# Optimization experiments

Measured on AMD Instinct MI355X. Metric: run time of the kernel, lower is better.

## Reference

```python
import jax, jax.numpy as jnp
import numpy as np

N = 8192      # number of tree nodes
K = 8         # max degree (8-ary tree)
ALPHA = 64    # alphabet size
DH = 256      # hidden dim


def _lin_w(key, din, dout):
    return jax.random.normal(key, (din, dout), jnp.float32) / np.sqrt(din)


def setup_inputs() -> dict:
    keys = jax.random.split(jax.random.key(0), 24)
    node_types = jax.random.randint(keys[0], (N,), 0, ALPHA, dtype=jnp.int32)
    # deterministic K-ary tree: children of node n are n*K+1 .. n*K+K (if < N)
    idx = np.arange(N)[:, None] * K + 1 + np.arange(K)[None, :]
    mask = idx < N
    children_np = np.where(mask, idx, 0).astype(np.int32)
    A_np = np.zeros((N, N), np.float32)
    A_np[np.repeat(np.arange(N), K)[mask.ravel()], idx.ravel()[mask.ravel()]] = 1.0
    return {
        "node_types": node_types,
        "children": jnp.asarray(children_np),
        "child_mask": jnp.asarray(mask),
        "A": jnp.asarray(A_np),
        # GCN layer params (self-transform + neighbor-transform)
        "Ws0": _lin_w(keys[1], ALPHA, DH), "Wn0": _lin_w(keys[2], ALPHA, DH), "b0": jnp.zeros((DH,), jnp.float32),
        "Ws1": _lin_w(keys[3], DH, DH),    "Wn1": _lin_w(keys[4], DH, DH),    "b1": jnp.zeros((DH,), jnp.float32),
        "Ws2": _lin_w(keys[5], DH, DH),    "Wn2": _lin_w(keys[6], DH, DH),    "b2": jnp.zeros((DH,), jnp.float32),
        # heads
        "we": _lin_w(keys[7], DH, 1), "be": jnp.zeros((1,), jnp.float32),
        "Wt": _lin_w(keys[8], DH, ALPHA), "bt": jnp.zeros((ALPHA,), jnp.float32),
        "ciu_w": _lin_w(keys[9], DH, 1)[:, 0], "ciu_b": jnp.zeros((), jnp.float32),
        "civ_w": _lin_w(keys[10], DH, 1)[:, 0], "civ_b": jnp.zeros((), jnp.float32),
        "ciw_w": jax.random.normal(keys[11], (), jnp.float32), "ciw_b": jnp.zeros((), jnp.float32),
        "cnu_w": _lin_w(keys[12], DH, 1)[:, 0], "cnu_b": jnp.zeros((), jnp.float32),
        "cnv_w": _lin_w(keys[13], DH, 1)[:, 0], "cnv_b": jnp.zeros((), jnp.float32),
        "cnw_w": jax.random.normal(keys[14], (), jnp.float32), "cnw_b": jnp.zeros((), jnp.float32),
    }


def reference(node_types, children, child_mask, A,
              Ws0, Wn0, b0, Ws1, Wn1, b1, Ws2, Wn2, b2,
              we, be, Wt, bt,
              ciu_w, ciu_b, civ_w, civ_b, ciw_w, ciw_b,
              cnu_w, cnu_b, cnv_w, cnv_b, cnw_w, cnw_b):
    X = jax.nn.one_hot(node_types, ALPHA, dtype=jnp.float32)  # [N, ALPHA]

    def gcn(Z, Ws, Wn, b):
        # self transform + adjacency-aggregated neighbor transform
        return Z @ Ws + b + A @ (Z @ Wn)

    H = jax.nn.relu(gcn(X, Ws0, Wn0, b0))
    H = jax.nn.relu(gcn(H, Ws1, Wn1, b1))
    H = jax.nn.relu(gcn(H, Ws2, Wn2, b2))  # [N, DH]

    delta = H @ we + be   # [N, 1] edit scores
    types = H @ Wt + bt   # [N, ALPHA]

    # child index / child num heads only for nodes with delta >= 0.5 and >0 children
    active = (delta[:, 0] >= 0.5) & child_mask.any(-1)
    valid = child_mask & active[:, None]          # [N, K]
    Hc = H[children]                               # [N, K, DH]
    dots = jnp.einsum('nkd,nd->nk', Hc, H)         # [N, K] child-parent products

    s_idx = (H @ ciu_w + ciu_b)[:, None] + (Hc @ civ_w + civ_b) + (ciw_w * dots + ciw_b)
    s_idx = jnp.where(valid, s_idx, 0.0)
    Cidx = jnp.zeros((N, K + 1), jnp.float32).at[:, 0].set(-1.0)
    # scores[i,1:deg+1] = s; scores[i,:deg] -= s  (s is zero-padded past deg)
    Cidx = Cidx.at[:, 1:].add(s_idx).at[:, :K].add(-s_idx)

    s_num = (H @ cnu_w + cnu_b)[:, None] + (Hc @ cnv_w + cnv_b) + (cnw_w * dots + cnw_b)
    Cnum = jnp.where(valid, s_num, 0.0)

    return delta, types, Cidx, Cnum
```

## Files before the change

### kernel.cpp

```cpp
#include <hip/hip_runtime.h>
#include <hip/hip_bf16.h>

#define N 8192
#define KDEG 8
#define ALPHA 64
#define DH 256

typedef unsigned short ushort_t;
typedef __attribute__((ext_vector_type(8))) short short8;
typedef __attribute__((ext_vector_type(4))) float f32x4;
typedef __attribute__((ext_vector_type(4))) unsigned short ushort4_t;

__device__ __forceinline__ float wave_reduce_sum(float v) {
#pragma unroll
    for (int off = 32; off > 0; off >>= 1) v += __shfl_xor(v, off, 64);
    return v;
}

__device__ __forceinline__ ushort_t bf16_of(float x) {
    __hip_bfloat16 h = __float2bfloat16(x);
    return *(ushort_t*)&h;
}
__device__ __forceinline__ float f_of_bf16(ushort_t u) {
    __hip_bfloat16 h = *(__hip_bfloat16*)&u;
    return __bfloat162float(h);
}

__global__ __launch_bounds__(256) void k_embed_pack(const int* __restrict__ nt,
                                                    const float* __restrict__ Ws0,
                                                    const float* __restrict__ Wn0,
                                                    const float* __restrict__ b0,
                                                    const float* __restrict__ W0,
                                                    const float* __restrict__ W1,
                                                    const float* __restrict__ W2,
                                                    const float* __restrict__ W3,
                                                    const float* __restrict__ W4,
                                                    ushort_t* __restrict__ Hhi,
                                                    ushort_t* __restrict__ Hlo,
                                                    ushort_t* __restrict__ Phi,
                                                    ushort_t* __restrict__ Plo) {
    if (blockIdx.x < 2048) {
        int g = blockIdx.x * 256 + threadIdx.x;
        int n = g >> 6, d = (g & 63) * 4;
        int t = nt[n];
        f32x4 acc = *(const f32x4*)(b0 + d);
        acc += *(const f32x4*)(Ws0 + t * DH + d);
        int cb = n * KDEG + 1;
#pragma unroll
        for (int k = 0; k < KDEG; k++) {
            int c = cb + k;
            if (c < N) acc += *(const f32x4*)(Wn0 + nt[c] * DH + d);
        }
        ushort4_t hi, lo;
#pragma unroll
        for (int i = 0; i < 4; i++) {
            float x = fmaxf(acc[i], 0.0f);
            ushort_t h = bf16_of(x);
            hi[i] = h;
            lo[i] = bf16_of(x - f_of_bf16(h));
        }
        *(ushort4_t*)(Hhi + (size_t)n * DH + d) = hi;
        *(ushort4_t*)(Hlo + (size_t)n * DH + d) = lo;
    } else {
        int e = (blockIdx.x - 2048) * 256 + threadIdx.x;
        if (e >= 262144 + 16384) return;
        const float* W;
        int o, Ncols;
        if (e < 262144) {
            int m = e >> 16; o = e & 65535; Ncols = 256;
            W = (m == 0) ? W0 : (m == 1) ? W1 : (m == 2) ? W2 : W3;
        } else {
            o = e - 262144; Ncols = 64; W = W4;
        }
        int j = o & 7, l = (o >> 3) & 63, r = o >> 9;
        int kb = r & 7, t = r >> 3;
        int k = kb * 32 + (l >> 4) * 8 + j;
        int c = t * 16 + (l & 15);
        float v = W[k * Ncols + c];
        ushort_t h = bf16_of(v);
        Phi[e] = h;
        Plo[e] = bf16_of(v - f_of_bf16(h));
    }
}

__global__ __launch_bounds__(256) void k_gemm(const ushort_t* __restrict__ Hhi,
                                              const ushort_t* __restrict__ Hlo,
                                              const ushort_t* __restrict__ PShi,
                                              const ushort_t* __restrict__ PSlo,
                                              const ushort_t* __restrict__ PNhi,
                                              const ushort_t* __restrict__ PNlo,
                                              float* __restrict__ S,
                                              float* __restrict__ M) {
    int w = blockIdx.x * 4 + (threadIdx.x >> 6);
    int lane = threadIdx.x & 63;
    int rg = w >> 3, mat = (w >> 2) & 1, cg = w & 3;
    const ushort_t* Bh = mat ? PNhi : PShi;
    const ushort_t* Bl = mat ? PNlo : PSlo;
    float* Out = mat ? M : S;
    int r0 = rg * 32, c0 = cg * 64;
    int mrow = lane & 15, quad = lane >> 4;

    f32x4 acc[2][4] = {};
    const ushort_t* ah0p = Hhi + (size_t)(r0 + mrow) * DH + quad * 8;
    const ushort_t* al0p = Hlo + (size_t)(r0 + mrow) * DH + quad * 8;
#pragma unroll
    for (int kb = 0; kb < 8; kb++) {
        short8 ah0 = *(const short8*)(ah0p + kb * 32);
        short8 ah1 = *(const short8*)(ah0p + 16 * DH + kb * 32);
        short8 al0 = *(const short8*)(al0p + kb * 32);
        short8 al1 = *(const short8*)(al0p + 16 * DH + kb * 32);
#pragma unroll
        for (int ct = 0; ct < 4; ct++) {
            int t = cg * 4 + ct;
            const ushort_t* bp = Bh + (size_t)((t * 8 + kb) * 64 + lane) * 8;
            const ushort_t* lp = Bl + (size_t)((t * 8 + kb) * 64 + lane) * 8;
            short8 bh = *(const short8*)bp;
            short8 bl = *(const short8*)lp;
            acc[0][ct] = __builtin_amdgcn_mfma_f32_16x16x32_bf16(ah0, bh, acc[0][ct], 0, 0, 0);
            acc[1][ct] = __builtin_amdgcn_mfma_f32_16x16x32_bf16(ah1, bh, acc[1][ct], 0, 0, 0);
            acc[0][ct] = __builtin_amdgcn_mfma_f32_16x16x32_bf16(ah0, bl, acc[0][ct], 0, 0, 0);
            acc[1][ct] = __builtin_amdgcn_mfma_f32_16x16x32_bf16(ah1, bl, acc[1][ct], 0, 0, 0);
            acc[0][ct] = __builtin_amdgcn_mfma_f32_16x16x32_bf16(al0, bh, acc[0][ct], 0, 0, 0);
            acc[1][ct] = __builtin_amdgcn_mfma_f32_16x16x32_bf16(al1, bh, acc[1][ct], 0, 0, 0);
        }
    }
#pragma unroll
    for (int rt = 0; rt < 2; rt++)
#pragma unroll
        for (int ct = 0; ct < 4; ct++) {
            int col = c0 + ct * 16 + mrow;
            int rowb = r0 + rt * 16 + quad * 4;
#pragma unroll
            for (int r = 0; r < 4; r++)
                Out[(size_t)(rowb + r) * DH + col] = acc[rt][ct][r];
        }
}

template <bool WITH_SCALARS>
__global__ __launch_bounds__(256) void k_combine(const float* __restrict__ S,
                                                 const float* __restrict__ M,
                                                 const float* __restrict__ b,
                                                 ushort_t* __restrict__ Hhi,
                                                 ushort_t* __restrict__ Hlo,
                                                 const float* __restrict__ we,
                                                 const float* __restrict__ be,
                                                 const float* __restrict__ ciu_w,
                                                 const float* __restrict__ ciu_b,
                                                 const float* __restrict__ civ_w,
                                                 const float* __restrict__ civ_b,
                                                 const float* __restrict__ cnu_w,
                                                 const float* __restrict__ cnu_b,
                                                 const float* __restrict__ cnv_w,
                                                 const float* __restrict__ cnv_b,
                                                 float* __restrict__ aux,
                                                 float* __restrict__ delta_out) {
    int g = blockIdx.x * 256 + threadIdx.x;
    int n = g >> 6, j = g & 63, d = j * 4;
    f32x4 acc = *(const f32x4*)(S + (size_t)n * DH + d);
    acc += *(const f32x4*)(b + d);
    int cb = n * KDEG + 1;
#pragma unroll
    for (int k = 0; k < KDEG; k++) {
        int c = cb + k;
        if (c < N) acc += *(const f32x4*)(M + (size_t)c * DH + d);
    }
    f32x4 x;
    ushort4_t hi, lo;
#pragma unroll
    for (int i = 0; i < 4; i++) {
        x[i] = fmaxf(acc[i], 0.0f);
        ushort_t h = bf16_of(x[i]);
        hi[i] = h;
        lo[i] = bf16_of(x[i] - f_of_bf16(h));
    }
    *(ushort4_t*)(Hhi + (size_t)n * DH + d) = hi;
    *(ushort4_t*)(Hlo + (size_t)n * DH + d) = lo;

    if (WITH_SCALARS) {
        f32x4 w0 = *(const f32x4*)(we + d);
        f32x4 w1 = *(const f32x4*)(ciu_w + d);
        f32x4 w2 = *(const f32x4*)(civ_w + d);
        f32x4 w3 = *(const f32x4*)(cnu_w + d);
        f32x4 w4 = *(const f32x4*)(cnv_w + d);
        float pd = 0.f, p1 = 0.f, p2 = 0.f, p3 = 0.f, p4 = 0.f;
#pragma unroll
        for (int i = 0; i < 4; i++) {
            pd += x[i] * w0[i];
            p1 += x[i] * w1[i];
            p2 += x[i] * w2[i];
            p3 += x[i] * w3[i];
            p4 += x[i] * w4[i];
        }
        pd = wave_reduce_sum(pd);
        p1 = wave_reduce_sum(p1);
        p2 = wave_reduce_sum(p2);
        p3 = wave_reduce_sum(p3);
        p4 = wave_reduce_sum(p4);
        if (j == 0) {
            float dv = pd + be[0];
            aux[n * 8 + 0] = dv;
            aux[n * 8 + 1] = p1 + ciu_b[0];
            aux[n * 8 + 2] = p2 + civ_b[0];
            aux[n * 8 + 3] = p3 + cnu_b[0];
            aux[n * 8 + 4] = p4 + cnv_b[0];
            delta_out[n] = dv;
        }
    }
}

__global__ __launch_bounds__(256) void k_heads(const ushort_t* __restrict__ Hhi,
                                               const ushort_t* __restrict__ Hlo,
                                               const ushort_t* __restrict__ Bh,
                                               const ushort_t* __restrict__ Bl,
                                               const float* __restrict__ bt,
                                               const float* __restrict__ aux,
                                               const float* __restrict__ ciw_w,
                                               const float* __restrict__ ciw_b,
                                               const float* __restrict__ cnw_w,
                                               const float* __restrict__ cnw_b,
                                               float* __restrict__ types_out,
                                               float* __restrict__ cidx_out,
                                               float* __restrict__ cnum_out) {
    int lane = threadIdx.x & 63;
    if (blockIdx.x < 128) {
        int w = blockIdx.x * 4 + (threadIdx.x >> 6);
        int mrow = lane & 15, quad = lane >> 4;
        int r0 = w * 16;
        f32x4 acc[4] = {};
        const ushort_t* ap = Hhi + (size_t)(r0 + mrow) * DH + quad * 8;
        const ushort_t* lp = Hlo + (size_t)(r0 + mrow) * DH + quad * 8;
#pragma unroll
        for (int kb = 0; kb < 8; kb++) {
            short8 ah = *(const short8*)(ap + kb * 32);
            short8 al = *(const short8*)(lp + kb * 32);
#pragma unroll
            for (int ct = 0; ct < 4; ct++) {
                short8 bh = *(const short8*)(Bh + (size_t)((ct * 8 + kb) * 64 + lane) * 8);
                short8 bl = *(const short8*)(Bl + (size_t)((ct * 8 + kb) * 64 + lane) * 8);
                acc[ct] = __builtin_amdgcn_mfma_f32_16x16x32_bf16(ah, bh, acc[ct], 0, 0, 0);
                acc[ct] = __builtin_amdgcn_mfma_f32_16x16x32_bf16(ah, bl, acc[ct], 0, 0, 0);
                acc[ct] = __builtin_amdgcn_mfma_f32_16x16x32_bf16(al, bh, acc[ct], 0, 0, 0);
            }
        }
#pragma unroll
        for (int ct = 0; ct < 4; ct++) {
            float bias = bt[ct * 16 + mrow];
            int rowb = r0 + quad * 4;
#pragma unroll
            for (int r = 0; r < 4; r++)
                types_out[(size_t)(rowb + r) * ALPHA + ct * 16 + mrow] = acc[ct][r] + bias;
        }
    } else {
        int n = (blockIdx.x - 128) * 4 + (threadIdx.x >> 6);
        int j = lane, d = j * 4;
        ushort4_t phi = *(const ushort4_t*)(Hhi + (size_t)n * DH + d);
        ushort4_t plo = *(const ushort4_t*)(Hlo + (size_t)n * DH + d);
        float hp[4];
#pragma unroll
        for (int i = 0; i < 4; i++) hp[i] = f_of_bf16(phi[i]) + f_of_bf16(plo[i]);

        float delta = aux[n * 8 + 0];
        bool active = (delta >= 0.5f) && (n * KDEG + 1 < N);
        float ciu_n = aux[n * 8 + 1];
        float cnu_n = aux[n * 8 + 3];
        float iw = ciw_w[0], ib = ciw_b[0], nw = cnw_w[0], nb = cnw_b[0];

        float my_si = 0.f, my_sn = 0.f;
#pragma unroll
        for (int k = 0; k < KDEG; k++) {
            int c = n * KDEG + 1 + k;
            float si = 0.f, sn = 0.f;
            if (c < N) {
                ushort4_t chi = *(const ushort4_t*)(Hhi + (size_t)c * DH + d);
                ushort4_t clo = *(const ushort4_t*)(Hlo + (size_t)c * DH + d);
                float p = 0.f;
#pragma unroll
                for (int i = 0; i < 4; i++)
                    p += hp[i] * (f_of_bf16(chi[i]) + f_of_bf16(clo[i]));
                p = wave_reduce_sum(p);
                if (active) {
                    si = ciu_n + aux[c * 8 + 2] + iw * p + ib;
                    sn = cnu_n + aux[c * 8 + 4] + nw * p + nb;
                }
            }
            if (j == k) { my_si = si; my_sn = sn; }
        }
        if (j < KDEG) cnum_out[(size_t)n * KDEG + j] = my_sn;
        float prev = __shfl(my_si, (j >= 1) ? (j - 1) : 0, 64);
        float val;
        if (j == 0)        val = -1.f - my_si;
        else if (j < KDEG) val = prev - my_si;
        else               val = prev;
        if (j <= KDEG) cidx_out[(size_t)n * (KDEG + 1) + j] = val;
    }
}

extern "C" void kernel_launch(void* const* d_in, const int* in_sizes, int n_in,
                              void* d_out, int out_size, void* d_ws, size_t ws_size,
                              hipStream_t stream) {
    const int* nt = (const int*)d_in[0];
    const float* Ws0 = (const float*)d_in[4];
    const float* Wn0 = (const float*)d_in[5];
    const float* b0  = (const float*)d_in[6];
    const float* Ws1 = (const float*)d_in[7];
    const float* Wn1 = (const float*)d_in[8];
    const float* b1  = (const float*)d_in[9];
    const float* Ws2 = (const float*)d_in[10];
    const float* Wn2 = (const float*)d_in[11];
    const float* b2  = (const float*)d_in[12];
    const float* we  = (const float*)d_in[13];
    const float* be  = (const float*)d_in[14];
    const float* Wt  = (const float*)d_in[15];
    const float* bt  = (const float*)d_in[16];
    const float* ciu_w = (const float*)d_in[17];
    const float* ciu_b = (const float*)d_in[18];
    const float* civ_w = (const float*)d_in[19];
    const float* civ_b = (const float*)d_in[20];
    const float* ciw_w = (const float*)d_in[21];
    const float* ciw_b = (const float*)d_in[22];
    const float* cnu_w = (const float*)d_in[23];
    const float* cnu_b = (const float*)d_in[24];
    const float* cnv_w = (const float*)d_in[25];
    const float* cnv_b = (const float*)d_in[26];
    const float* cnw_w = (const float*)d_in[27];
    const float* cnw_b = (const float*)d_in[28];

    char* w = (char*)d_ws;
    float*    S   = (float*)(w);
    float*    M   = (float*)(w + ((size_t)8  << 20));
    float*    aux = (float*)(w + ((size_t)16 << 20));
    ushort_t* Hhi = (ushort_t*)(w + ((size_t)17 << 20));
    ushort_t* Hlo = (ushort_t*)(w + ((size_t)21 << 20));
    ushort_t* Phi = (ushort_t*)(w + ((size_t)25 << 20));
    ushort_t* Plo = (ushort_t*)(w + ((size_t)26 << 20));

    float* delta_out = (float*)d_out;
    float* types_out = delta_out + N;
    float* cidx_out  = types_out + (size_t)N * ALPHA;
    float* cnum_out  = cidx_out + (size_t)N * (KDEG + 1);

    k_embed_pack<<<3136, 256, 0, stream>>>(nt, Ws0, Wn0, b0,
                                           Ws1, Wn1, Ws2, Wn2, Wt,
                                           Hhi, Hlo, Phi, Plo);
    k_gemm<<<512, 256, 0, stream>>>(Hhi, Hlo, Phi, Plo, Phi + 65536, Plo + 65536, S, M);
    k_combine<false><<<2048, 256, 0, stream>>>(S, M, b1, Hhi, Hlo,
                                               nullptr, nullptr, nullptr, nullptr, nullptr,
                                               nullptr, nullptr, nullptr, nullptr, nullptr,
                                               nullptr, nullptr);
    k_gemm<<<512, 256, 0, stream>>>(Hhi, Hlo, Phi + 131072, Plo + 131072,
                                    Phi + 196608, Plo + 196608, S, M);
    k_combine<true><<<2048, 256, 0, stream>>>(S, M, b2, Hhi, Hlo,
                                              we, be, ciu_w, ciu_b, civ_w, civ_b,
                                              cnu_w, cnu_b, cnv_w, cnv_b, aux, delta_out);
    k_heads<<<128 + 2048, 256, 0, stream>>>(Hhi, Hlo, Phi + 262144, Plo + 262144, bt,
                                            aux, ciw_w, ciw_b, cnw_w, cnw_b,
                                            types_out, cidx_out, cnum_out);
}
```

Measured before the change: 410.6 us.

## Fuse GCN combine into GEMM via aggregate-first K=512 concat formulation

The per-layer GCN moves from a separate S/M GEMM followed by a combine kernel to one K=512 GEMM over [H | A·H], with weights [Ws; Wn] packed together. Each block computes 64 consecutive rows that are exactly the children of 8 parents, so the next layer's child-sum aggregate is built in shared memory within the same kernel. Bias, relu, the hi/lo bf16 split and the scalar head dot products (via atomics into aux) also move into the epilogue. This cuts two launches and the fp32 S/M round trips through global memory, but there are only 256 GEMM blocks, the root node needs a special single block, and atomics into aux need a zeroing pass.

```diff
diff --git a/kernel.cpp b/kernel.cpp
--- a/kernel.cpp
+++ b/kernel.cpp
@@ -6,116 +6,212 @@
 #define ALPHA 64
 #define DH 256
 
-typedef unsigned short ushort_t;
+typedef unsigned short u16;
 typedef __attribute__((ext_vector_type(8))) short short8;
 typedef __attribute__((ext_vector_type(4))) float f32x4;
 typedef __attribute__((ext_vector_type(4))) unsigned short ushort4_t;
+typedef __attribute__((ext_vector_type(8))) unsigned short ushort8_t;
 
 __device__ __forceinline__ float wave_reduce_sum(float v) {
 #pragma unroll
     for (int off = 32; off > 0; off >>= 1) v += __shfl_xor(v, off, 64);
     return v;
 }
-
-__device__ __forceinline__ ushort_t bf16_of(float x) {
+__device__ __forceinline__ u16 bf16_of(float x) {
     __hip_bfloat16 h = __float2bfloat16(x);
-    return *(ushort_t*)&h;
-}
-__device__ __forceinline__ float f_of_bf16(ushort_t u) {
+    return *(u16*)&h;
+}
+__device__ __forceinline__ float f_of_bf16(u16 u) {
     __hip_bfloat16 h = *(__hip_bfloat16*)&u;
     return __bfloat162float(h);
 }
 
+
 __global__ __launch_bounds__(256) void k_embed_pack(const int* __restrict__ nt,
-                                                    const float* __restrict__ Ws0,
-                                                    const float* __restrict__ Wn0,
-                                                    const float* __restrict__ b0,
-                                                    const float* __restrict__ W0,
-                                                    const float* __restrict__ W1,
-                                                    const float* __restrict__ W2,
-                                                    const float* __restrict__ W3,
-                                                    const float* __restrict__ W4,
-                                                    ushort_t* __restrict__ Hhi,
-                                                    ushort_t* __restrict__ Hlo,
-                                                    ushort_t* __restrict__ Phi,
-                                                    ushort_t* __restrict__ Plo) {
-    if (blockIdx.x < 2048) {
-        int g = blockIdx.x * 256 + threadIdx.x;
-        int n = g >> 6, d = (g & 63) * 4;
-        int t = nt[n];
-        f32x4 acc = *(const f32x4*)(b0 + d);
-        acc += *(const f32x4*)(Ws0 + t * DH + d);
-        int cb = n * KDEG + 1;
-#pragma unroll
-        for (int k = 0; k < KDEG; k++) {
-            int c = cb + k;
-            if (c < N) acc += *(const f32x4*)(Wn0 + nt[c] * DH + d);
-        }
-        ushort4_t hi, lo;
+    const float* __restrict__ Ws0, const float* __restrict__ Wn0, const float* __restrict__ b0,
+    const float* __restrict__ Ws1, const float* __restrict__ Wn1,
+    const float* __restrict__ Ws2, const float* __restrict__ Wn2,
+    const float* __restrict__ Wt,
+    u16* __restrict__ H0hi, u16* __restrict__ H0lo,
+    u16* __restrict__ A0hi, u16* __restrict__ A0lo,
+    u16* __restrict__ Phi, u16* __restrict__ Plo,
+    float* __restrict__ aux) {
+    int tid = threadIdx.x;
+    if (blockIdx.x < 128) {
+        __shared__ float X[64][260];
+        int t = blockIdx.x, r0 = 64 * t + 1;
+        for (int u = 0; u < 16; u++) {
+            int uid = tid + 256 * u;
+            int lr = uid >> 6, d = (uid & 63) * 4;
+            int row = r0 + lr;
+            if (row < N) {
+                f32x4 a = *(const f32x4*)(b0 + d);
+                a += *(const f32x4*)(Ws0 + nt[row] * DH + d);
+                int cb = row * KDEG + 1;
+#pragma unroll
+                for (int i = 0; i < KDEG; i++) {
+                    int c = cb + i;
+                    if (c < N) a += *(const f32x4*)(Wn0 + nt[c] * DH + d);
+                }
+                ushort4_t hi, lo;
+                f32x4 x;
+#pragma unroll
+                for (int i = 0; i < 4; i++) {
+                    x[i] = fmaxf(a[i], 0.f);
+                    u16 h = bf16_of(x[i]);
+                    hi[i] = h;
+                    lo[i] = bf16_of(x[i] - f_of_bf16(h));
+                }
+                *(ushort4_t*)(H0hi + (size_t)row * DH + d) = hi;
+                *(ushort4_t*)(H0lo + (size_t)row * DH + d) = lo;
+                *(f32x4*)&X[lr][d] = x;
+            }
+        }
+        __syncthreads();
+        int node = 8 * t + (tid >> 5);
+        int c8 = (tid & 31) * 8;
+        f32x4 s0 = {}, s1 = {};
+#pragma unroll
+        for (int i = 0; i < KDEG; i++) {
+            int lr = (tid >> 5) * 8 + i;
+            if (r0 + lr < N) {
+                s0 += *(f32x4*)&X[lr][c8];
+                s1 += *(f32x4*)&X[lr][c8 + 4];
+            }
+        }
+        ushort8_t hi, lo;
 #pragma unroll
         for (int i = 0; i < 4; i++) {
-            float x = fmaxf(acc[i], 0.0f);
-            ushort_t h = bf16_of(x);
-            hi[i] = h;
-            lo[i] = bf16_of(x - f_of_bf16(h));
-        }
-        *(ushort4_t*)(Hhi + (size_t)n * DH + d) = hi;
-        *(ushort4_t*)(Hlo + (size_t)n * DH + d) = lo;
+            u16 h0 = bf16_of(s0[i]); hi[i] = h0;     lo[i] = bf16_of(s0[i] - f_of_bf16(h0));
+            u16 h1 = bf16_of(s1[i]); hi[4 + i] = h1; lo[4 + i] = bf16_of(s1[i] - f_of_bf16(h1));
+        }
+        *(ushort8_t*)(A0hi + (size_t)node * DH + c8) = hi;
+        *(ushort8_t*)(A0lo + (size_t)node * DH + c8) = lo;
+    } else if (blockIdx.x == 128) {
+        if (tid < 64) {
+            int d = tid * 4;
+            f32x4 a = *(const f32x4*)(b0 + d);
+            a += *(const f32x4*)(Ws0 + nt[0] * DH + d);
+#pragma unroll
+            for (int i = 1; i <= KDEG; i++) a += *(const f32x4*)(Wn0 + nt[i] * DH + d);
+            ushort4_t hi, lo;
+#pragma unroll
+            for (int i = 0; i < 4; i++) {
+                float x = fmaxf(a[i], 0.f);
+                u16 h = bf16_of(x);
+                hi[i] = h;
+                lo[i] = bf16_of(x - f_of_bf16(h));
+            }
+            *(ushort4_t*)(H0hi + d) = hi;
+            *(ushort4_t*)(H0lo + d) = lo;
+        } else if (tid < 192) {
+            int c = (tid - 64) * 2;
+            A0hi[(size_t)1024 * DH + c] = 0; A0hi[(size_t)1024 * DH + c + 1] = 0;
+            A0lo[(size_t)1024 * DH + c] = 0; A0lo[(size_t)1024 * DH + c + 1] = 0;
+        }
     } else {
-        int e = (blockIdx.x - 2048) * 256 + threadIdx.x;
-        if (e >= 262144 + 16384) return;
-        const float* W;
-        int o, Ncols;
+        int e = (blockIdx.x - 129) * 256 + tid;
         if (e < 262144) {
-            int m = e >> 16; o = e & 65535; Ncols = 256;
-            W = (m == 0) ? W0 : (m == 1) ? W1 : (m == 2) ? W2 : W3;
-        } else {
-            o = e - 262144; Ncols = 64; W = W4;
-        }
-        int j = o & 7, l = (o >> 3) & 63, r = o >> 9;
-        int kb = r & 7, t = r >> 3;
-        int k = kb * 32 + (l >> 4) * 8 + j;
-        int c = t * 16 + (l & 15);
-        float v = W[k * Ncols + c];
-        ushort_t h = bf16_of(v);
-        Phi[e] = h;
-        Plo[e] = bf16_of(v - f_of_bf16(h));
-    }
-}
-
-__global__ __launch_bounds__(256) void k_gemm(const ushort_t* __restrict__ Hhi,
-                                              const ushort_t* __restrict__ Hlo,
-                                              const ushort_t* __restrict__ PShi,
-                                              const ushort_t* __restrict__ PSlo,
-                                              const ushort_t* __restrict__ PNhi,
-                                              const ushort_t* __restrict__ PNlo,
-                                              float* __restrict__ S,
-                                              float* __restrict__ M) {
-    int w = blockIdx.x * 4 + (threadIdx.x >> 6);
-    int lane = threadIdx.x & 63;
-    int rg = w >> 3, mat = (w >> 2) & 1, cg = w & 3;
-    const ushort_t* Bh = mat ? PNhi : PShi;
-    const ushort_t* Bl = mat ? PNlo : PSlo;
-    float* Out = mat ? M : S;
-    int r0 = rg * 32, c0 = cg * 64;
+            int m = e >> 17, o = e & 131071;
+            int j = o & 7, l = (o >> 3) & 63, r = o >> 9;
+            int kb = r & 15, tt = r >> 4;
+            int k = kb * 32 + (l >> 4) * 8 + j;
+            int c = tt * 16 + (l & 15);
+            const float* W = (k < 256) ? (m ? Ws2 : Ws1) : (m ? Wn2 : Wn1);
+            float v = W[(k & 255) * DH + c];
+            u16 h = bf16_of(v);
+            Phi[e] = h;
+            Plo[e] = bf16_of(v - f_of_bf16(h));
+        } else if (e < 278528) {
+            int o = e - 262144;
+            int j = o & 7, l = (o >> 3) & 63, r = o >> 9;
+            int kb = r & 7, tt = r >> 3;
+            int k = kb * 32 + (l >> 4) * 8 + j;
+            int c = tt * 16 + (l & 15);
+            float v = Wt[k * ALPHA + c];
+            u16 h = bf16_of(v);
+            Phi[e] = h;
+            Plo[e] = bf16_of(v - f_of_bf16(h));
+        } else if (e < 278528 + 65536) {
+            aux[e - 278528] = 0.f;
+        }
+    }
+}
+
+template <bool AGG, bool SCAL>
+__global__ __launch_bounds__(256) void k_gemm(
+    const u16* __restrict__ Hhi, const u16* __restrict__ Hlo,
+    const u16* __restrict__ Aghi, const u16* __restrict__ Aglo,
+    const u16* __restrict__ Pmhi, const u16* __restrict__ Pmlo,
+    const float* __restrict__ bias,
+    u16* __restrict__ Ohi, u16* __restrict__ Olo,
+    u16* __restrict__ AOhi, u16* __restrict__ AOlo,
+    const float* __restrict__ we, const float* __restrict__ ciu_w,
+    const float* __restrict__ civ_w, const float* __restrict__ cnu_w,
+    const float* __restrict__ cnv_w, float* __restrict__ aux) {
+    int tid = threadIdx.x;
+    if (blockIdx.x == 256) {
+        __shared__ float G[512];
+        int c = tid;
+        G[c] = f_of_bf16(Hhi[c]) + f_of_bf16(Hlo[c]);
+        G[c + 256] = f_of_bf16(Aghi[c]) + f_of_bf16(Aglo[c]);
+        if (AGG) { AOhi[(size_t)1024 * DH + c] = 0; AOlo[(size_t)1024 * DH + c] = 0; }
+        __syncthreads();
+        float z = bias[c];
+        for (int k = 0; k < 512; k++) {
+            int idx = (((c >> 4) * 16 + (k >> 5)) * 64 + ((k >> 3) & 3) * 16 + (c & 15)) * 8 + (k & 7);
+            z += G[k] * (f_of_bf16(Pmhi[idx]) + f_of_bf16(Pmlo[idx]));
+        }
+        float x = fmaxf(z, 0.f);
+        u16 h = bf16_of(x);
+        Ohi[c] = h;
+        Olo[c] = bf16_of(x - f_of_bf16(h));
+        if (SCAL) {
+            float p0 = wave_reduce_sum(x * we[c]);
+            float p1 = wave_reduce_sum(x * ciu_w[c]);
+            float p2 = wave_reduce_sum(x * civ_w[c]);
+            float p3 = wave_reduce_sum(x * cnu_w[c]);
+            float p4 = wave_reduce_sum(x * cnv_w[c]);
+            if ((tid & 63) == 0) {
+                atomicAdd(&aux[0], p0); atomicAdd(&aux[1], p1); atomicAdd(&aux[2], p2);
+                atomicAdd(&aux[3], p3); atomicAdd(&aux[4], p4);
+            }
+        }
+        return;
+    }
+    __shared__ float X[64][132];
+    int b = blockIdx.x;
+    int t = b >> 1, cg = b & 1;
+    int r0 = 64 * t + 1, c0 = cg * 128;
+    int lane = tid & 63, wave = tid >> 6;
+    int wr = wave >> 1, wc = wave & 1;
     int mrow = lane & 15, quad = lane >> 4;
+    int rb = r0 + wr * 32;
+    bool full = (t < 16);
+
+    int ar0 = rb + mrow;        if (ar0 > N - 1) ar0 = N - 1;
+    int ar1 = rb + 16 + mrow;   if (ar1 > N - 1) ar1 = N - 1;
+    const u16* h0h = Hhi + (size_t)ar0 * DH + quad * 8;
+    const u16* h0l = Hlo + (size_t)ar0 * DH + quad * 8;
+    const u16* h1h = Hhi + (size_t)ar1 * DH + quad * 8;
+    const u16* h1l = Hlo + (size_t)ar1 * DH + quad * 8;
+    const u16* g0h = Aghi + (size_t)ar0 * DH + quad * 8;
+    const u16* g0l = Aglo + (size_t)ar0 * DH + quad * 8;
+    const u16* g1h = Aghi + (size_t)ar1 * DH + quad * 8;
+    const u16* g1l = Aglo + (size_t)ar1 * DH + quad * 8;
 
     f32x4 acc[2][4] = {};
-    const ushort_t* ah0p = Hhi + (size_t)(r0 + mrow) * DH + quad * 8;
-    const ushort_t* al0p = Hlo + (size_t)(r0 + mrow) * DH + quad * 8;
-#pragma unroll
-    for (int kb = 0; kb < 8; kb++) {
-        short8 ah0 = *(const short8*)(ah0p + kb * 32);
-        short8 ah1 = *(const short8*)(ah0p + 16 * DH + kb * 32);
-        short8 al0 = *(const short8*)(al0p + kb * 32);
-        short8 al1 = *(const short8*)(al0p + 16 * DH + kb * 32);
+    auto kstep = [&](int ka, const u16* p0h, const u16* p0l,
+                     const u16* p1h, const u16* p1l, int kbB) {
+        short8 ah0 = *(const short8*)(p0h + ka * 32);
+        short8 al0 = *(const short8*)(p0l + ka * 32);
+        short8 ah1 = *(const short8*)(p1h + ka * 32);
+        short8 al1 = *(const short8*)(p1l + ka * 32);
 #pragma unroll
         for (int ct = 0; ct < 4; ct++) {
-            int t = cg * 4 + ct;
-            const ushort_t* bp = Bh + (size_t)((t * 8 + kb) * 64 + lane) * 8;
-            const ushort_t* lp = Bl + (size_t)((t * 8 + kb) * 64 + lane) * 8;
-            short8 bh = *(const short8*)bp;
-            short8 bl = *(const short8*)lp;
+            size_t bo = ((size_t)((cg * 8 + wc * 4 + ct) * 16 + kbB) * 64 + lane) * 8;
+            short8 bh = *(const short8*)(Pmhi + bo);
+            short8 bl = *(const short8*)(Pmlo + bo);
             acc[0][ct] = __builtin_amdgcn_mfma_f32_16x16x32_bf16(ah0, bh, acc[0][ct], 0, 0, 0);
             acc[1][ct] = __builtin_amdgcn_mfma_f32_16x16x32_bf16(ah1, bh, acc[1][ct], 0, 0, 0);
             acc[0][ct] = __builtin_amdgcn_mfma_f32_16x16x32_bf16(ah0, bl, acc[0][ct], 0, 0, 0);
@@ -123,101 +219,105 @@
             acc[0][ct] = __builtin_amdgcn_mfma_f32_16x16x32_bf16(al0, bh, acc[0][ct], 0, 0, 0);
             acc[1][ct] = __builtin_amdgcn_mfma_f32_16x16x32_bf16(al1, bh, acc[1][ct], 0, 0, 0);
         }
+    };
+#pragma unroll
+    for (int kb = 0; kb < 8; kb++) kstep(kb, h0h, h0l, h1h, h1l, kb);
+    if (full) {
+#pragma unroll
+        for (int kb = 0; kb < 8; kb++) kstep(kb, g0h, g0l, g1h, g1l, kb + 8);
     }
 #pragma unroll
     for (int rt = 0; rt < 2; rt++)
 #pragma unroll
         for (int ct = 0; ct < 4; ct++) {
-            int col = c0 + ct * 16 + mrow;
-            int rowb = r0 + rt * 16 + quad * 4;
-#pragma unroll
-            for (int r = 0; r < 4; r++)
-                Out[(size_t)(rowb + r) * DH + col] = acc[rt][ct][r];
-        }
-}
-
-template <bool WITH_SCALARS>
-__global__ __launch_bounds__(256) void k_combine(const float* __restrict__ S,
-                                                 const float* __restrict__ M,
-                                                 const float* __restrict__ b,
-                                                 ushort_t* __restrict__ Hhi,
-                                                 ushort_t* __restrict__ Hlo,
-                                                 const float* __restrict__ we,
-                                                 const float* __restrict__ be,
-                                                 const float* __restrict__ ciu_w,
-                                                 const float* __restrict__ ciu_b,
-                                                 const float* __restrict__ civ_w,
-                                                 const float* __restrict__ civ_b,
-                                                 const float* __restrict__ cnu_w,
-                                                 const float* __restrict__ cnu_b,
-                                                 const float* __restrict__ cnv_w,
-                                                 const float* __restrict__ cnv_b,
-                                                 float* __restrict__ aux,
-                                                 float* __restrict__ delta_out) {
-    int g = blockIdx.x * 256 + threadIdx.x;
-    int n = g >> 6, j = g & 63, d = j * 4;
-    f32x4 acc = *(const f32x4*)(S + (size_t)n * DH + d);
-    acc += *(const f32x4*)(b + d);
-    int cb = n * KDEG + 1;
-#pragma unroll
-    for (int k = 0; k < KDEG; k++) {
-        int c = cb + k;
-        if (c < N) acc += *(const f32x4*)(M + (size_t)c * DH + d);
-    }
-    f32x4 x;
-    ushort4_t hi, lo;
-#pragma unroll
-    for (int i = 0; i < 4; i++) {
-        x[i] = fmaxf(acc[i], 0.0f);
-        ushort_t h = bf16_of(x[i]);
-        hi[i] = h;
-        lo[i] = bf16_of(x[i] - f_of_bf16(h));
-    }
-    *(ushort4_t*)(Hhi + (size_t)n * DH + d) = hi;
-    *(ushort4_t*)(Hlo + (size_t)n * DH + d) = lo;
-
-    if (WITH_SCALARS) {
-        f32x4 w0 = *(const f32x4*)(we + d);
-        f32x4 w1 = *(const f32x4*)(ciu_w + d);
-        f32x4 w2 = *(const f32x4*)(civ_w + d);
-        f32x4 w3 = *(const f32x4*)(cnu_w + d);
-        f32x4 w4 = *(const f32x4*)(cnv_w + d);
-        float pd = 0.f, p1 = 0.f, p2 = 0.f, p3 = 0.f, p4 = 0.f;
+            int col = wc * 64 + ct * 16 + mrow;
+            float bb = bias[c0 + col];
+#pragma unroll
+            for (int r = 0; r < 4; r++) {
+                int lrow = wr * 32 + rt * 16 + quad * 4 + r;
+                X[lrow][col] = fmaxf(acc[rt][ct][r] + bb, 0.f);
+            }
+        }
+    __syncthreads();
+    {
+        int lrow = tid >> 2, cs = (tid & 3) * 32;
+        int grow = r0 + lrow;
+        if (grow < N) {
+#pragma unroll
+            for (int s = 0; s < 4; s++) {
+                f32x4 x0 = *(f32x4*)&X[lrow][cs + s * 8];
+                f32x4 x1 = *(f32x4*)&X[lrow][cs + s * 8 + 4];
+                ushort8_t hi, lo;
+#pragma unroll
+                for (int i = 0; i < 4; i++) {
+                    u16 h0 = bf16_of(x0[i]); hi[i] = h0;     lo[i] = bf16_of(x0[i] - f_of_bf16(h0));
+                    u16 h1 = bf16_of(x1[i]); hi[4 + i] = h1; lo[4 + i] = bf16_of(x1[i] - f_of_bf16(h1));
+                }
+                *(ushort8_t*)(Ohi + (size_t)grow * DH + c0 + cs + s * 8) = hi;
+                *(ushort8_t*)(Olo + (size_t)grow * DH + c0 + cs + s * 8) = lo;
+            }
+        }
+        if (SCAL) {
+            float p[5] = {0.f, 0.f, 0.f, 0.f, 0.f};
+            if (grow < N) {
+                for (int c = 0; c < 32; c++) {
+                    float x = X[lrow][cs + c];
+                    int col = c0 + cs + c;
+                    p[0] += x * we[col];
+                    p[1] += x * ciu_w[col];
+                    p[2] += x * civ_w[col];
+                    p[3] += x * cnu_w[col];
+                    p[4] += x * cnv_w[col];
+                }
+            }
+#pragma unroll
+            for (int h = 0; h < 5; h++) {
+                p[h] += __shfl_xor(p[h], 1, 64);
+                p[h] += __shfl_xor(p[h], 2, 64);
+            }
+            if ((tid & 3) == 0 && grow < N) {
+#pragma unroll
+                for (int h = 0; h < 5; h++) atomicAdd(&aux[grow * 8 + h], p[h]);
+            }
+        }
+    }
+    if (AGG) {
+        int node = 8 * t + (tid >> 5);
+        int c4 = (tid & 31) * 4;
+        f32x4 s = {};
+#pragma unroll
+        for (int i = 0; i < KDEG; i++) {
+            int lr = (tid >> 5) * 8 + i;
+            if (r0 + lr < N) s += *(f32x4*)&X[lr][c4];
+        }
+        ushort4_t hi, lo;
 #pragma unroll
         for (int i = 0; i < 4; i++) {
-            pd += x[i] * w0[i];
-            p1 += x[i] * w1[i];
-            p2 += x[i] * w2[i];
-            p3 += x[i] * w3[i];
-            p4 += x[i] * w4[i];
-        }
-        pd = wave_reduce_sum(pd);
-        p1 = wave_reduce_sum(p1);
-        p2 = wave_reduce_sum(p2);
-        p3 = wave_reduce_sum(p3);
-        p4 = wave_reduce_sum(p4);
-        if (j == 0) {
-            float dv = pd + be[0];
-            aux[n * 8 + 0] = dv;
-            aux[n * 8 + 1] = p1 + ciu_b[0];
-            aux[n * 8 + 2] = p2 + civ_b[0];
-            aux[n * 8 + 3] = p3 + cnu_b[0];
-            aux[n * 8 + 4] = p4 + cnv_b[0];
-            delta_out[n] = dv;
-        }
-    }
-}
-
-__global__ __launch_bounds__(256) void k_heads(const ushort_t* __restrict__ Hhi,
-                                               const ushort_t* __restrict__ Hlo,
-                                               const ushort_t* __restrict__ Bh,
-                                               const ushort_t* __restrict__ Bl,
+            u16 h = bf16_of(s[i]);
+            hi[i] = h;
+            lo[i] = bf16_of(s[i] - f_of_bf16(h));
+        }
+        *(ushort4_t*)(AOhi + (size_t)node * DH + c0 + c4) = hi;
+        *(ushort4_t*)(AOlo + (size_t)node * DH + c0 + c4) = lo;
+    }
+}
+
+__global__ __launch_bounds__(256) void k_heads(const u16* __restrict__ Hhi,
+                                               const u16* __restrict__ Hlo,
+                                               const u16* __restrict__ Bh,
+                                               const u16* __restrict__ Bl,
                                                const float* __restrict__ bt,
                                                const float* __restrict__ aux,
+                                               const float* __restrict__ be,
+                                               const float* __restrict__ ciu_b,
+                                               const float* __restrict__ civ_b,
                                                const float* __restrict__ ciw_w,
                                                const float* __restrict__ ciw_b,
+                                               const float* __restrict__ cnu_b,
+                                               const float* __restrict__ cnv_b,
                                                const float* __restrict__ cnw_w,
                                                const float* __restrict__ cnw_b,
+                                               float* __restrict__ delta_out,
                                                float* __restrict__ types_out,
                                                float* __restrict__ cidx_out,
                                                float* __restrict__ cnum_out) {
@@ -227,8 +327,8 @@
         int mrow = lane & 15, quad = lane >> 4;
         int r0 = w * 16;
         f32x4 acc[4] = {};
-        const ushort_t* ap = Hhi + (size_t)(r0 + mrow) * DH + quad * 8;
-        const ushort_t* lp = Hlo + (size_t)(r0 + mrow) * DH + quad * 8;
+        const u16* ap = Hhi + (size_t)(r0 + mrow) * DH + quad * 8;
+        const u16* lp = Hlo + (size_t)(r0 + mrow) * DH + quad * 8;
 #pragma unroll
         for (int kb = 0; kb < 8; kb++) {
             short8 ah = *(const short8*)(ap + kb * 32);
@@ -259,11 +359,13 @@
 #pragma unroll
         for (int i = 0; i < 4; i++) hp[i] = f_of_bf16(phi[i]) + f_of_bf16(plo[i]);
 
-        float delta = aux[n * 8 + 0];
+        float delta = aux[n * 8 + 0] + be[0];
         bool active = (delta >= 0.5f) && (n * KDEG + 1 < N);
-        float ciu_n = aux[n * 8 + 1];
-        float cnu_n = aux[n * 8 + 3];
+        float ciu_n = aux[n * 8 + 1] + ciu_b[0];
+        float cnu_n = aux[n * 8 + 3] + cnu_b[0];
+        float cvb = civ_b[0], nvb = cnv_b[0];
         float iw = ciw_w[0], ib = ciw_b[0], nw = cnw_w[0], nb = cnw_b[0];
+        if (j == 0) delta_out[n] = delta;
 
         float my_si = 0.f, my_sn = 0.f;
 #pragma unroll
@@ -279,8 +381,8 @@
                     p += hp[i] * (f_of_bf16(chi[i]) + f_of_bf16(clo[i]));
                 p = wave_reduce_sum(p);
                 if (active) {
-                    si = ciu_n + aux[c * 8 + 2] + iw * p + ib;
-                    sn = cnu_n + aux[c * 8 + 4] + nw * p + nb;
+                    si = ciu_n + (aux[c * 8 + 2] + cvb) + iw * p + ib;
+                    sn = cnu_n + (aux[c * 8 + 4] + nvb) + nw * p + nb;
                 }
             }
             if (j == k) { my_si = si; my_sn = sn; }
@@ -326,33 +428,37 @@
     const float* cnw_b = (const float*)d_in[28];
 
     char* w = (char*)d_ws;
-    float*    S   = (float*)(w);
-    float*    M   = (float*)(w + ((size_t)8  << 20));
-    float*    aux = (float*)(w + ((size_t)16 << 20));
-    ushort_t* Hhi = (ushort_t*)(w + ((size_t)17 << 20));
-    ushort_t* Hlo = (ushort_t*)(w + ((size_t)21 << 20));
-    ushort_t* Phi = (ushort_t*)(w + ((size_t)25 << 20));
-    ushort_t* Plo = (ushort_t*)(w + ((size_t)26 << 20));
+    u16* H0hi = (u16*)(w);
+    u16* H0lo = (u16*)(w + ((size_t)4 << 20));
+    u16* A0hi = (u16*)(w + ((size_t)8 << 20));
+    u16* A0lo = (u16*)(w + ((size_t)12 << 20));
+    u16* H1hi = (u16*)(w + ((size_t)16 << 20));
+    u16* H1lo = (u16*)(w + ((size_t)20 << 20));
+    u16* A1hi = (u16*)(w + ((size_t)24 << 20));
+    u16* A1lo = (u16*)(w + ((size_t)28 << 20));
+    u16* H2hi = (u16*)(w + ((size_t)32 << 20));
+    u16* H2lo = (u16*)(w + ((size_t)36 << 20));
+    float* aux = (float*)(w + ((size_t)40 << 20));
+    u16* Phi = (u16*)(w + ((size_t)41 << 20));
+    u16* Plo = (u16*)(w + ((size_t)42 << 20));
 
     float* delta_out = (float*)d_out;
     float* types_out = delta_out + N;
     float* cidx_out  = types_out + (size_t)N * ALPHA;
     float* cnum_out  = cidx_out + (size_t)N * (KDEG + 1);
 
-    k_embed_pack<<<3136, 256, 0, stream>>>(nt, Ws0, Wn0, b0,
-                                           Ws1, Wn1, Ws2, Wn2, Wt,
-                                           Hhi, Hlo, Phi, Plo);
-    k_gemm<<<512, 256, 0, stream>>>(Hhi, Hlo, Phi, Plo, Phi + 65536, Plo + 65536, S, M);
-    k_combine<false><<<2048, 256, 0, stream>>>(S, M, b1, Hhi, Hlo,
-                                               nullptr, nullptr, nullptr, nullptr, nullptr,
-                                               nullptr, nullptr, nullptr, nullptr, nullptr,
-                                               nullptr, nullptr);
-    k_gemm<<<512, 256, 0, stream>>>(Hhi, Hlo, Phi + 131072, Plo + 131072,
-                                    Phi + 196608, Plo + 196608, S, M);
-    k_combine<true><<<2048, 256, 0, stream>>>(S, M, b2, Hhi, Hlo,
-                                              we, be, ciu_w, ciu_b, civ_w, civ_b,
-                                              cnu_w, cnu_b, cnv_w, cnv_b, aux, delta_out);
-    k_heads<<<128 + 2048, 256, 0, stream>>>(Hhi, Hlo, Phi + 262144, Plo + 262144, bt,
-                                            aux, ciw_w, ciw_b, cnw_w, cnw_b,
-                                            types_out, cidx_out, cnum_out);
-}
+    k_embed_pack<<<1473, 256, 0, stream>>>(nt, Ws0, Wn0, b0, Ws1, Wn1, Ws2, Wn2, Wt,
+                                           H0hi, H0lo, A0hi, A0lo, Phi, Plo, aux);
+    k_gemm<true, false><<<257, 256, 0, stream>>>(H0hi, H0lo, A0hi, A0lo,
+                                                 Phi, Plo, b1, H1hi, H1lo, A1hi, A1lo,
+                                                 nullptr, nullptr, nullptr, nullptr, nullptr,
+                                                 nullptr);
+    k_gemm<false, true><<<257, 256, 0, stream>>>(H1hi, H1lo, A1hi, A1lo,
+                                                 Phi + 131072, Plo + 131072, b2,
+                                                 H2hi, H2lo, nullptr, nullptr,
+                                                 we, ciu_w, civ_w, cnu_w, cnv_w, aux);
+    k_heads<<<128 + 2048, 256, 0, stream>>>(H2hi, H2lo, Phi + 262144, Plo + 262144, bt,
+                                            aux, be, ciu_b, civ_b, ciw_w, ciw_b,
+                                            cnu_b, cnv_b, cnw_w, cnw_b,
+                                            delta_out, types_out, cidx_out, cnum_out);
+}
```

After: 530.3 us. 1.29x slower.
